# Kernel optimization log

Hardware: AMD Instinct MI355X
Metric: run time of the kernel (lower is better)

The kernel has to match this reference:

```python
import jax, jax.numpy as jnp
import numpy as np

EPS = 1e-08

def setup_inputs() -> dict:
    key = jax.random.key(0)
    k1, k2, k3, k4 = jax.random.split(key, 4)
    batch, n_in, n_out, D = 32768, 256, 512, 16
    x = jax.random.uniform(k1, (batch, n_in), jnp.float32, minval=-1.0, maxval=1.0)
    omega = jax.random.normal(k2, (D, 1), jnp.float32)          # stddev=1.0 init
    phase = 0.1 * jax.random.normal(k3, (D, 1), jnp.float32)    # zeros in module; small noise for non-degenerate test
    std_c = 1.0 / np.sqrt(n_in * D)
    c_basis = std_c * jax.random.normal(k4, (n_out, n_in, D), jnp.float32)
    bias = jnp.zeros((n_out,), jnp.float32)
    return {"x": x, "omega": omega, "phase": phase, "c_basis": c_basis, "bias": bias}

def _basis(x, omega, phase):
    # x: (batch, n_in) -> B: (batch, n_in, D)
    D = omega.shape[0]
    w = omega.reshape(1, 1, D)
    p = phase.reshape(1, 1, D)
    wx = w * x[..., None]
    s = jnp.sin(wx + p)
    mu = jnp.exp(-0.5 * w ** 2) * jnp.sin(p)
    std = jnp.sqrt(0.5 * (1.0 - jnp.exp(-2.0 * w ** 2) * jnp.cos(2.0 * p)) - mu ** 2)
    return (s + mu) / (std + EPS)

def reference(x, omega, phase, c_basis, bias):
    B = _basis(x, omega, phase)                     # (batch, n_in, D)
    y = jnp.einsum('bid,oid->bo', B, c_basis)       # (batch, n_out)
    return y + bias
```

## Files before the change

### kernel.cpp

```cpp
#include <hip/hip_runtime.h>
#include <hip/hip_bf16.h>


#define BATCH 32768
#define NIN   256
#define NOUT  512
#define DDIM  16
#define BM    128
#define BN    512
#define BK    64
#define NKT   ((NIN*DDIM)/BK)
#define TILE_BYTES (BN*BK*2)
#define ABYTES (BM*BK*2)
#define BBYTES (BN*BK*2)
#define EPSV  1e-8f
#define INV2PI 0.15915494309189535f

typedef short  bf16x8 __attribute__((ext_vector_type(8)));
typedef float  f32x4  __attribute__((ext_vector_type(4)));

static __device__ __forceinline__ ushort f2bf(float f) {
  union { __hip_bfloat16 h; ushort u; } cv;
  cv.h = __float2bfloat16(f);
  return cv.u;
}

static __device__ __forceinline__ float sgpr_f(float v) {
  return __builtin_bit_cast(float,
      __builtin_amdgcn_readfirstlane(__builtin_bit_cast(int, v)));
}

__global__ __launch_bounds__(256) void prep_kernel(
    const float* __restrict__ omega, const float* __restrict__ phase,
    const float* __restrict__ c_basis, const float* __restrict__ bias,
    ushort* __restrict__ cb, float* __restrict__ offs)
{
  __shared__ float s_scale[DDIM];
  __shared__ float s_musc[DDIM];
  __shared__ float s_red[4];

  const int o = blockIdx.x;
  const int t = threadIdx.x;

  if (t < DDIM) {
    float w = omega[t];
    float p = phase[t];
    float mu  = expf(-0.5f * w * w) * sinf(p);
    float var = 0.5f * (1.0f - expf(-2.0f * w * w) * cosf(2.0f * p)) - mu * mu;
    float sd  = sqrtf(fmaxf(var, 0.0f));
    float sc  = 1.0f / (sd + EPSV);
    s_scale[t] = sc;
    s_musc[t]  = mu * sc;
  }
  __syncthreads();

  const float* cp = c_basis + ((size_t)o * NIN + t) * DDIM;
  float cv[DDIM];
  {
    const float4* cp4 = (const float4*)cp;
    float4 a = cp4[0], b = cp4[1], c = cp4[2], d = cp4[3];
    cv[0]=a.x; cv[1]=a.y; cv[2]=a.z; cv[3]=a.w;
    cv[4]=b.x; cv[5]=b.y; cv[6]=b.z; cv[7]=b.w;
    cv[8]=c.x; cv[9]=c.y; cv[10]=c.z; cv[11]=c.w;
    cv[12]=d.x; cv[13]=d.y; cv[14]=d.z; cv[15]=d.w;
  }

  float partial = 0.0f;
  uint pk[8];
#pragma unroll
  for (int d = 0; d < DDIM; d += 2) {
    partial += cv[d] * s_musc[d] + cv[d+1] * s_musc[d+1];
    ushort u0 = f2bf(cv[d]   * s_scale[d]);
    ushort u1 = f2bf(cv[d+1] * s_scale[d+1]);
    pk[d >> 1] = (uint)u0 | ((uint)u1 << 16);
  }

  {
    const int r   = o;
    const int kt  = t >> 2;
    const int swz = (r & 7) << 4;
    char* tile = (char*)cb + (size_t)kt * TILE_BYTES;
    int b0 = r * 128 + (t & 3) * 32;
    *(uint4*)(tile + ((b0     ) ^ swz)) = make_uint4(pk[0], pk[1], pk[2], pk[3]);
    *(uint4*)(tile + ((b0 + 16) ^ swz)) = make_uint4(pk[4], pk[5], pk[6], pk[7]);
  }

#pragma unroll
  for (int off = 32; off > 0; off >>= 1) partial += __shfl_down(partial, off, 64);
  if ((t & 63) == 0) s_red[t >> 6] = partial;
  __syncthreads();
  if (t == 0) offs[o] = bias[o] + s_red[0] + s_red[1] + s_red[2] + s_red[3];
}

__global__ __launch_bounds__(512, 2) void gemm_kernel(
    const float* __restrict__ x, const float* __restrict__ omega,
    const float* __restrict__ phase, const ushort* __restrict__ cb,
    const float* __restrict__ offs, float* __restrict__ out)
{
  extern __shared__ char lds[];

  const int t    = threadIdx.x;
  const int lane = t & 63;
  const int wid  = t >> 6;
  const int wm   = wid >> 2;
  const int wn   = wid & 3;
  const int row0 = blockIdx.x * BM;

  float wv[DDIM], pv[DDIM];
#pragma unroll
  for (int d = 0; d < DDIM; ++d) {
    wv[d] = sgpr_f(omega[d] * INV2PI);
    pv[d] = sgpr_f(phase[d] * INV2PI);
  }

  f32x4 acc[4][8];
#pragma unroll
  for (int m = 0; m < 4; ++m)
#pragma unroll
    for (int n = 0; n < 8; ++n) acc[m][n] = (f32x4){0.f, 0.f, 0.f, 0.f};

  const int arow = t >> 2;
  const int acol = t & 3;
  const float* xbase = x + (size_t)(row0 + arow) * NIN + acol;
  const int aswz = (arow & 7) << 4;
  const int ab0  = arow * 128 + acol * 32;

  const int hi  = lane >> 4;
  const int l15 = lane & 15;

#define GLL(s_, d_) __builtin_amdgcn_global_load_lds(                          \
      (const __attribute__((address_space(1))) void*)(s_),                     \
      (__attribute__((address_space(3))) void*)(d_), 16, 0, 0)

#define ISSUE_B(kt_, sb_)                                                      \
  {                                                                            \
    const char* src = (const char*)cb + (size_t)(kt_) * TILE_BYTES             \
                      + wid * 8192 + lane * 16;                                \
    char* dst = lds + 32768 + (sb_) * BBYTES + wid * 8192;                     \
    GLL(src, dst);                 GLL(src + 1024, dst + 1024);                \
    GLL(src + 2048, dst + 2048);   GLL(src + 3072, dst + 3072);                \
    GLL(src + 4096, dst + 4096);   GLL(src + 5120, dst + 5120);                \
    GLL(src + 6144, dst + 6144);   GLL(src + 7168, dst + 7168);                \
  }

#define STAGE_A(xx_, sb_)                                                      \
  {                                                                            \
    char* AsB = lds + (sb_) * ABYTES;                                          \
    uint pk[8];                                                                \
    _Pragma("unroll")                                                          \
    for (int d = 0; d < DDIM; d += 2) {                                        \
      float s0 = __builtin_amdgcn_sinf(fmaf(wv[d],   (xx_), pv[d]));           \
      float s1 = __builtin_amdgcn_sinf(fmaf(wv[d+1], (xx_), pv[d+1]));         \
      uint u0 = __builtin_bit_cast(uint, s0) + 0x8000u;                        \
      uint u1 = __builtin_bit_cast(uint, s1) + 0x8000u;                        \
      pk[d >> 1] = __builtin_amdgcn_perm(u1, u0, 0x07060302u);                 \
    }                                                                          \
    *(uint4*)(AsB + ((ab0     ) ^ aswz)) = make_uint4(pk[0],pk[1],pk[2],pk[3]);\
    *(uint4*)(AsB + ((ab0 + 16) ^ aswz)) = make_uint4(pk[4],pk[5],pk[6],pk[7]);\
  }

#define MFMA_STEP(mb_)                                                         \
  {                                                                            \
    const char* AsB = lds + (mb_) * ABYTES;                                    \
    const char* BsB = lds + 32768 + (mb_) * BBYTES;                            \
    __builtin_amdgcn_s_setprio(1);                                             \
    _Pragma("unroll")                                                          \
    for (int kk = 0; kk < 2; ++kk) {                                           \
      bf16x8 af[4];                                                            \
      _Pragma("unroll")                                                        \
      for (int m = 0; m < 4; ++m) {                                            \
        int rr = wm * 64 + m * 16 + l15;                                       \
        af[m] = *(const bf16x8*)(AsB + ((rr*128 + kk*64 + hi*16) ^ ((rr&7)<<4))); \
      }                                                                        \
      _Pragma("unroll")                                                        \
      for (int nh = 0; nh < 2; ++nh) {                                         \
        bf16x8 bfr[4];                                                         \
        _Pragma("unroll")                                                      \
        for (int n4 = 0; n4 < 4; ++n4) {                                       \
          int rr = wn * 128 + (nh * 4 + n4) * 16 + l15;                        \
          bfr[n4] = *(const bf16x8*)(BsB + ((rr*128 + kk*64 + hi*16) ^ ((rr&7)<<4))); \
        }                                                                      \
        _Pragma("unroll")                                                      \
        for (int m = 0; m < 4; ++m)                                            \
          _Pragma("unroll")                                                    \
          for (int n4 = 0; n4 < 4; ++n4)                                       \
            acc[m][nh * 4 + n4] = __builtin_amdgcn_mfma_f32_16x16x32_bf16(     \
                af[m], bfr[n4], acc[m][nh * 4 + n4], 0, 0, 0);                 \
      }                                                                        \
    }                                                                          \
    __builtin_amdgcn_s_setprio(0);                                             \
  }

#define CBAR(vm_)                                                              \
  __builtin_amdgcn_sched_barrier(0);                                           \
  asm volatile("s_waitcnt vmcnt(" #vm_ ") lgkmcnt(0)" ::: "memory");           \
  __builtin_amdgcn_s_barrier();                                                \
  __builtin_amdgcn_sched_barrier(0);

#define BODY(kt_, mb_, sb_, XU_, XL_)                                          \
  {                                                                            \
    ISSUE_B(((kt_) + 1 < NKT ? (kt_) + 1 : NKT - 1), sb_);                     \
    __builtin_amdgcn_sched_barrier(0);                                         \
    XL_ = xbase[((kt_) + 2 < NKT ? (kt_) + 2 : NKT - 1) * 4];                  \
    __builtin_amdgcn_sched_barrier(0);                                         \
    STAGE_A(XU_, sb_);                                                         \
    __builtin_amdgcn_sched_barrier(0);                                         \
    MFMA_STEP(mb_);                                                            \
    CBAR(1)                                                                    \
  }

  float xs0, xs1;
  {
    float xp = xbase[0];
    __builtin_amdgcn_sched_barrier(0);
    ISSUE_B(0, 0);
    __builtin_amdgcn_sched_barrier(0);
    xs1 = xbase[4];
    __builtin_amdgcn_sched_barrier(0);
    STAGE_A(xp, 0);
    CBAR(1)
  }

  for (int kt = 0; kt < NKT; kt += 2) {
    BODY(kt,     0, 1, xs1, xs0)
    BODY(kt + 1, 1, 0, xs0, xs1)
  }

#pragma unroll
  for (int n = 0; n < 8; ++n) {
    int col = wn * 128 + n * 16 + l15;
    float off = offs[col];
#pragma unroll
    for (int m = 0; m < 4; ++m) {
      int row = row0 + wm * 64 + m * 16 + hi * 4;
      float* op = out + (size_t)row * NOUT + col;
#pragma unroll
      for (int j = 0; j < 4; ++j)
        op[(size_t)j * NOUT] = acc[m][n][j] + off;
    }
  }
}

extern "C" void kernel_launch(void* const* d_in, const int* in_sizes, int n_in,
                              void* d_out, int out_size, void* d_ws, size_t ws_size,
                              hipStream_t stream) {
  const float* x       = (const float*)d_in[0];
  const float* omega   = (const float*)d_in[1];
  const float* phase   = (const float*)d_in[2];
  const float* c_basis = (const float*)d_in[3];
  const float* bias    = (const float*)d_in[4];
  float* out = (float*)d_out;

  float*  offs = (float*)d_ws;
  ushort* cb   = (ushort*)((char*)d_ws + 2048);

  hipFuncSetAttribute((const void*)gemm_kernel,
                      hipFuncAttributeMaxDynamicSharedMemorySize, 163840);

  prep_kernel<<<NOUT, 256, 0, stream>>>(omega, phase, c_basis, bias, cb, offs);
  gemm_kernel<<<BATCH / BM, 512, 163840, stream>>>(x, omega, phase, cb, offs, out);
}
```

Before: 142.2 us.

## Split each K-step into four barrier-delimited phases interleaving loads, sin, and MFMA

Each K-tile body is restructured into four phases. Every phase issues a quarter of the next B tile's global-to-LDS loads, part of the sin basis computation for A, and the LDS fragment reads, then runs one MFMA quarter between s_barriers. The aim is a ping-pong style schedule that keeps MFMA, VALU transcendental and memory work overlapped instead of running them back-to-back. The cost is more barriers per tile, and the vmcnt accounting may not account for all in-flight loads.

```diff
diff --git a/kernel.cpp b/kernel.cpp
--- a/kernel.cpp
+++ b/kernel.cpp
@@ -132,93 +132,117 @@
       (const __attribute__((address_space(1))) void*)(s_),                     \
       (__attribute__((address_space(3))) void*)(d_), 16, 0, 0)
 
-#define ISSUE_B(kt_, sb_)                                                      \
+#define ISSUE_B2(kt_, sb_, q_)                                                 \
   {                                                                            \
     const char* src = (const char*)cb + (size_t)(kt_) * TILE_BYTES             \
-                      + wid * 8192 + lane * 16;                                \
-    char* dst = lds + 32768 + (sb_) * BBYTES + wid * 8192;                     \
-    GLL(src, dst);                 GLL(src + 1024, dst + 1024);                \
-    GLL(src + 2048, dst + 2048);   GLL(src + 3072, dst + 3072);                \
-    GLL(src + 4096, dst + 4096);   GLL(src + 5120, dst + 5120);                \
-    GLL(src + 6144, dst + 6144);   GLL(src + 7168, dst + 7168);                \
-  }
-
-#define STAGE_A(xx_, sb_)                                                      \
-  {                                                                            \
-    char* AsB = lds + (sb_) * ABYTES;                                          \
-    uint pk[8];                                                                \
-    _Pragma("unroll")                                                          \
-    for (int d = 0; d < DDIM; d += 2) {                                        \
+                      + wid * 8192 + (q_) * 2048 + lane * 16;                  \
+    char* dst = lds + 32768 + (sb_) * BBYTES + wid * 8192 + (q_) * 2048;       \
+    GLL(src, dst); GLL(src + 1024, dst + 1024);                                \
+  }
+
+#define SINS_HALF(xx_, h_)                                                     \
+    _Pragma("unroll")                                                          \
+    for (int d = (h_) * 8; d < (h_) * 8 + 8; d += 2) {                         \
       float s0 = __builtin_amdgcn_sinf(fmaf(wv[d],   (xx_), pv[d]));           \
       float s1 = __builtin_amdgcn_sinf(fmaf(wv[d+1], (xx_), pv[d+1]));         \
       uint u0 = __builtin_bit_cast(uint, s0) + 0x8000u;                        \
       uint u1 = __builtin_bit_cast(uint, s1) + 0x8000u;                        \
       pk[d >> 1] = __builtin_amdgcn_perm(u1, u0, 0x07060302u);                 \
-    }                                                                          \
-    *(uint4*)(AsB + ((ab0     ) ^ aswz)) = make_uint4(pk[0],pk[1],pk[2],pk[3]);\
-    *(uint4*)(AsB + ((ab0 + 16) ^ aswz)) = make_uint4(pk[4],pk[5],pk[6],pk[7]);\
-  }
-
-#define MFMA_STEP(mb_)                                                         \
+    }
+
+#define A_WRITE(h_, sb_)                                                       \
+    *(uint4*)(lds + (sb_) * ABYTES + ((ab0 + (h_) * 16) ^ aswz)) =             \
+        make_uint4(pk[(h_)*4], pk[(h_)*4+1], pk[(h_)*4+2], pk[(h_)*4+3]);
+
+#define LOAD_AF(kk_)                                                           \
+    _Pragma("unroll")                                                          \
+    for (int m = 0; m < 4; ++m) {                                              \
+      int rr = wm * 64 + m * 16 + l15;                                         \
+      af[m] = *(const bf16x8*)(AsB + ((rr*128 + (kk_)*64 + hi*16) ^ ((rr&7)<<4))); \
+    }
+
+#define LOAD_BF(kk_, nh_)                                                      \
+    _Pragma("unroll")                                                          \
+    for (int n4 = 0; n4 < 4; ++n4) {                                           \
+      int rr = wn * 128 + ((nh_) * 4 + n4) * 16 + l15;                         \
+      bfq[n4] = *(const bf16x8*)(BsB + ((rr*128 + (kk_)*64 + hi*16) ^ ((rr&7)<<4))); \
+    }
+
+#define MFMA_Q(kk_, nh_)                                                       \
+    __builtin_amdgcn_s_setprio(1);                                             \
+    _Pragma("unroll")                                                          \
+    for (int m = 0; m < 4; ++m)                                                \
+      _Pragma("unroll")                                                        \
+      for (int n4 = 0; n4 < 4; ++n4)                                           \
+        acc[m][(nh_)*4 + n4] = __builtin_amdgcn_mfma_f32_16x16x32_bf16(        \
+            af[m], bfq[n4], acc[m][(nh_)*4 + n4], 0, 0, 0);                    \
+    __builtin_amdgcn_s_setprio(0);
+
+#define PH_PRE                                                                 \
+    __builtin_amdgcn_sched_barrier(0);                                         \
+    __builtin_amdgcn_s_barrier();                                              \
+    asm volatile("s_waitcnt lgkmcnt(0)" ::: "memory");                         \
+    __builtin_amdgcn_sched_barrier(0);
+
+#define PH_POST                                                                \
+    __builtin_amdgcn_sched_barrier(0);                                         \
+    __builtin_amdgcn_s_barrier();                                              \
+    __builtin_amdgcn_sched_barrier(0);
+
+#define BODY(kt_, mb_, sb_, XU_, XL_)                                          \
   {                                                                            \
     const char* AsB = lds + (mb_) * ABYTES;                                    \
     const char* BsB = lds + 32768 + (mb_) * BBYTES;                            \
-    __builtin_amdgcn_s_setprio(1);                                             \
-    _Pragma("unroll")                                                          \
-    for (int kk = 0; kk < 2; ++kk) {                                           \
-      bf16x8 af[4];                                                            \
-      _Pragma("unroll")                                                        \
-      for (int m = 0; m < 4; ++m) {                                            \
-        int rr = wm * 64 + m * 16 + l15;                                       \
-        af[m] = *(const bf16x8*)(AsB + ((rr*128 + kk*64 + hi*16) ^ ((rr&7)<<4))); \
-      }                                                                        \
-      _Pragma("unroll")                                                        \
-      for (int nh = 0; nh < 2; ++nh) {                                         \
-        bf16x8 bfr[4];                                                         \
-        _Pragma("unroll")                                                      \
-        for (int n4 = 0; n4 < 4; ++n4) {                                       \
-          int rr = wn * 128 + (nh * 4 + n4) * 16 + l15;                        \
-          bfr[n4] = *(const bf16x8*)(BsB + ((rr*128 + kk*64 + hi*16) ^ ((rr&7)<<4))); \
-        }                                                                      \
-        _Pragma("unroll")                                                      \
-        for (int m = 0; m < 4; ++m)                                            \
-          _Pragma("unroll")                                                    \
-          for (int n4 = 0; n4 < 4; ++n4)                                       \
-            acc[m][nh * 4 + n4] = __builtin_amdgcn_mfma_f32_16x16x32_bf16(     \
-                af[m], bfr[n4], acc[m][nh * 4 + n4], 0, 0, 0);                 \
-      }                                                                        \
-    }                                                                          \
-    __builtin_amdgcn_s_setprio(0);                                             \
-  }
-
-#define CBAR(vm_)                                                              \
-  __builtin_amdgcn_sched_barrier(0);                                           \
-  asm volatile("s_waitcnt vmcnt(" #vm_ ") lgkmcnt(0)" ::: "memory");           \
-  __builtin_amdgcn_s_barrier();                                                \
-  __builtin_amdgcn_sched_barrier(0);
-
-#define BODY(kt_, mb_, sb_, XU_, XL_)                                          \
-  {                                                                            \
-    ISSUE_B(((kt_) + 1 < NKT ? (kt_) + 1 : NKT - 1), sb_);                     \
-    __builtin_amdgcn_sched_barrier(0);                                         \
+    const int ktn = ((kt_) + 1 < NKT ? (kt_) + 1 : NKT - 1);                   \
+    bf16x8 af[4], bfq[4];                                                      \
+    uint pk[8];                                                                \
+                                                                       \
+    ISSUE_B2(ktn, sb_, 0)                                                      \
+    LOAD_AF(0) LOAD_BF(0, 0)                                                   \
+    PH_PRE MFMA_Q(0, 0) PH_POST                                                \
+                                                                       \
+    ISSUE_B2(ktn, sb_, 1)                                                      \
+    LOAD_BF(0, 1)                                                              \
+    PH_PRE MFMA_Q(0, 1) PH_POST                                                \
+                                                                       \
+    ISSUE_B2(ktn, sb_, 2)                                                      \
+    SINS_HALF(XU_, 0)                                                          \
+    LOAD_AF(1) LOAD_BF(1, 0)                                                   \
+    PH_PRE MFMA_Q(1, 0)                                                        \
+    A_WRITE(0, sb_)                                                            \
+    PH_POST                                                                    \
+                                                                       \
+    ISSUE_B2(ktn, sb_, 3)                                                      \
+    SINS_HALF(XU_, 1)                                                          \
+    LOAD_BF(1, 1)                                                              \
     XL_ = xbase[((kt_) + 2 < NKT ? (kt_) + 2 : NKT - 1) * 4];                  \
-    __builtin_amdgcn_sched_barrier(0);                                         \
-    STAGE_A(XU_, sb_);                                                         \
-    __builtin_amdgcn_sched_barrier(0);                                         \
-    MFMA_STEP(mb_);                                                            \
-    CBAR(1)                                                                    \
+    PH_PRE MFMA_Q(1, 1)                                                        \
+    A_WRITE(1, sb_)                                                            \
+    __builtin_amdgcn_sched_barrier(0);                                         \
+    asm volatile("s_waitcnt vmcnt(1) lgkmcnt(0)" ::: "memory");                \
+    __builtin_amdgcn_s_barrier();                                              \
+    __builtin_amdgcn_sched_barrier(0);                                         \
   }
 
   float xs0, xs1;
   {
     float xp = xbase[0];
     __builtin_amdgcn_sched_barrier(0);
-    ISSUE_B(0, 0);
+    ISSUE_B2(0, 0, 0) ISSUE_B2(0, 0, 1) ISSUE_B2(0, 0, 2) ISSUE_B2(0, 0, 3)
     __builtin_amdgcn_sched_barrier(0);
     xs1 = xbase[4];
     __builtin_amdgcn_sched_barrier(0);
-    STAGE_A(xp, 0);
-    CBAR(1)
+    {
+      uint pk[8];
+      SINS_HALF(xp, 0)
+      SINS_HALF(xp, 1)
+      A_WRITE(0, 0)
+      A_WRITE(1, 0)
+    }
+    __builtin_amdgcn_sched_barrier(0);
+    asm volatile("s_waitcnt vmcnt(1) lgkmcnt(0)" ::: "memory");
+    __builtin_amdgcn_s_barrier();
+    __builtin_amdgcn_sched_barrier(0);
   }
 
   for (int kt = 0; kt < NKT; kt += 2) {
```

New measurement: 145.1 us. 1.02x slower.
